# Kernel tuning notes

Measured on AMD Instinct MI355X. Metric: run time of the kernel, lower is better.

Reference implementation:

```python
import jax, jax.numpy as jnp
import numpy as np

N = 50000      # nodes
E = 800000     # edges (avg degree 16)
IN = 128       # in_channels
OUT = 200      # out_channels


def setup_inputs() -> dict:
    key = jax.random.key(0)
    ks = jax.random.split(key, 12)
    x = jax.random.normal(ks[0], (N, IN), dtype=jnp.float32)
    src = jax.random.randint(ks[1], (E,), 0, N, dtype=jnp.int32)
    off = jax.random.randint(ks[2], (E,), 1, N, dtype=jnp.int32)
    dst = (src + off) % N  # guarantees no self-loops (PyG ChebConv removes them)
    edge_index = jnp.stack([src, dst])
    edge_weight = jax.random.uniform(ks[3], (E,), dtype=jnp.float32) + 0.1
    s = 0.05
    # scale_1 (K=1): one weight; scale_2 (K=2): two; scale_3 (K=3): three. Biases per scale.
    return {
        "x": x,
        "edge_index": edge_index,
        "edge_weight": edge_weight,
        "w1_0": jax.random.normal(ks[4], (IN, OUT), dtype=jnp.float32) * s,
        "b1": jnp.zeros((OUT,), dtype=jnp.float32),
        "w2_0": jax.random.normal(ks[5], (IN, OUT), dtype=jnp.float32) * s,
        "w2_1": jax.random.normal(ks[6], (IN, OUT), dtype=jnp.float32) * s,
        "b2": jnp.zeros((OUT,), dtype=jnp.float32),
        "w3_0": jax.random.normal(ks[7], (IN, OUT), dtype=jnp.float32) * s,
        "w3_1": jax.random.normal(ks[8], (IN, OUT), dtype=jnp.float32) * s,
        "w3_2": jax.random.normal(ks[9], (IN, OUT), dtype=jnp.float32) * s,
        "b3": jnp.zeros((OUT,), dtype=jnp.float32),
    }


def _cheb_norm(edge_index, edge_weight, num_nodes):
    # PyG ChebConv.__norm__ with normalization='sym', lambda_max=2.0:
    # L = I - D^{-1/2} A D^{-1/2}; Lhat = 2L/lambda_max - I = -D^{-1/2} A D^{-1/2}
    # (self-loop weights become exactly 0, so we can drop them)
    row, col = edge_index[0], edge_index[1]
    deg = jax.ops.segment_sum(edge_weight, row, num_segments=num_nodes)
    dis = jnp.where(deg > 0, jax.lax.rsqrt(deg), 0.0)
    return -dis[row] * edge_weight * dis[col]


def _propagate(h, src, dst, norm, num_nodes):
    # out[i] = sum_{(j->i) in E} norm_e * h[j]
    return jax.ops.segment_sum(norm[:, None] * h[src], dst, num_segments=num_nodes)


def reference(x, edge_index, edge_weight, w1_0, b1, w2_0, w2_1, b2, w3_0, w3_1, w3_2, b3):
    num_nodes = x.shape[0]
    src, dst = edge_index[0], edge_index[1]
    norm = _cheb_norm(edge_index, edge_weight, num_nodes)
    # Chebyshev recursion (shared across the three scales; identical math):
    tx0 = x                                              # T_0(L) x
    tx1 = _propagate(tx0, src, dst, norm, num_nodes)     # T_1(L) x = Lhat x
    tx2 = 2.0 * _propagate(tx1, src, dst, norm, num_nodes) - tx0  # T_2(L) x
    s1 = tx0 @ w1_0 + b1
    s2 = tx0 @ w2_0 + tx1 @ w2_1 + b2
    s3 = tx0 @ w3_0 + tx1 @ w3_1 + tx2 @ w3_2 + b3
    return (s1, s2, s3)
```

## Files before the change

kernel.cpp:

```cpp
#include <hip/hip_runtime.h>

#define IN 128
#define OUT 200
#define NT 13
#define MT 64
#define RANGES 8
#define REPLICAS 64
#define RBMAX 6272

typedef __bf16 bf16x8 __attribute__((ext_vector_type(8)));
typedef float f32x4 __attribute__((ext_vector_type(4)));
typedef unsigned short ushort;
typedef ushort ushort8 __attribute__((ext_vector_type(8)));
typedef unsigned int uint;

__device__ inline ushort f2bf(float f) {
  uint b = __float_as_uint(f);
  return (ushort)((b + 0x7FFFu + ((b >> 16) & 1u)) >> 16);
}
__device__ inline float bf_lo(uint v) { return __uint_as_float(v << 16); }
__device__ inline float bf_hi(uint v) { return __uint_as_float(v & 0xFFFF0000u); }

__device__ inline size_t pk_idx(int row, int ch) {
  int rt = row >> 4, lr = row & 15, kk = ch >> 5, hi = (ch & 31) >> 3;
  return ((size_t)(rt * 4 + kk) * 64 + hi * 16 + lr) * 8 + (ch & 7);
}

__device__ inline void gload16(const void* g, void* l) {
  __builtin_amdgcn_global_load_lds(
      (const __attribute__((address_space(1))) void*)g,
      (__attribute__((address_space(3))) void*)l, 16, 0, 0);
}


__global__ __launch_bounds__(256) void k_hist(
    const int* __restrict__ src, const int* __restrict__ dst,
    const float* __restrict__ w, float* __restrict__ deg_part,
    int* __restrict__ cnt_part, int E, int N, int RB, int SL) {
  __shared__ float degL[RBMAX];
  __shared__ int cntL[RBMAX];
  int range = blockIdx.x / REPLICAS;
  int rep = blockIdx.x % REPLICAS;
  int base = range * RB;
  int lim = min(N - base, RB);
  for (int i = threadIdx.x; i < RB; i += 256) { degL[i] = 0.f; cntL[i] = 0; }
  __syncthreads();
  int e0 = rep * SL, e1 = min(E, e0 + SL);
  for (int e = e0 + (int)threadIdx.x; e < e1; e += 256) {
    int s = src[e], d = dst[e];
    int sl = s - base, dl = d - base;
    if ((unsigned)sl < (unsigned)lim) atomicAdd(&degL[sl], w[e]);
    if ((unsigned)dl < (unsigned)lim) atomicAdd(&cntL[dl], 1);
  }
  __syncthreads();
  for (int i = threadIdx.x; i < lim; i += 256) {
    deg_part[(size_t)rep * N + base + i] = degL[i];
    cnt_part[(size_t)rep * N + base + i] = cntL[i];
  }
}

__global__ void k_dis_scan(const float* __restrict__ deg_part, int* __restrict__ cnt_part,
                           float* __restrict__ dis,
                           int* __restrict__ offs, int* __restrict__ bsum, int n) {
  __shared__ int s[256];
  int t = threadIdx.x;
  int i = blockIdx.x * 256 + t;
  int v = 0;
  if (i < n) {
    float d = 0.f;
    int run = 0;
    for (int c = 0; c < REPLICAS; ++c) {
      size_t idx = (size_t)c * n + i;
      int cv = cnt_part[idx];
      cnt_part[idx] = run;
      run += cv;
      d += deg_part[idx];
    }
    v = run;
    dis[i] = d > 0.f ? rsqrtf(d) : 0.f;
  }
  s[t] = v;
  __syncthreads();
  for (int o = 1; o < 256; o <<= 1) {
    int a = (t >= o) ? s[t - o] : 0;
    __syncthreads();
    s[t] += a;
    __syncthreads();
  }
  if (i < n) offs[i] = s[t] - v;
  if (t == 255) bsum[blockIdx.x] = s[255];
}

__global__ void k_scan_c2(int* __restrict__ offs, const int* __restrict__ bsum,
                          int n, int E) {
  __shared__ int red[256];
  int t = threadIdx.x;
  int partial = 0;
  for (int i = t; i < (int)blockIdx.x; i += 256) partial += bsum[i];
  red[t] = partial;
  __syncthreads();
  for (int o = 128; o > 0; o >>= 1) {
    if (t < o) red[t] += red[t + o];
    __syncthreads();
  }
  int base = red[0];
  int i = blockIdx.x * 256 + t;
  if (i < n) offs[i] += base;
  if (i == 0) offs[n] = E;
}

__global__ __launch_bounds__(256) void k_fill(
    const int* __restrict__ src, const int* __restrict__ dst,
    const float* __restrict__ w, const float* __restrict__ dis,
    const int* __restrict__ offs, const int* __restrict__ pref,
    int2* __restrict__ csr_rec, int E, int N, int RB, int SL) {
  __shared__ int curL[RBMAX];
  int range = blockIdx.x / REPLICAS;
  int rep = blockIdx.x % REPLICAS;
  int base = range * RB;
  int lim = min(N - base, RB);
  for (int i = threadIdx.x; i < RB; i += 256) curL[i] = 0;
  __syncthreads();
  int e0 = rep * SL, e1 = min(E, e0 + SL);
  for (int e = e0 + (int)threadIdx.x; e < e1; e += 256) {
    int d = dst[e];
    int dl = d - base;
    if ((unsigned)dl < (unsigned)lim) {
      int s = src[e];
      int r = atomicAdd(&curL[dl], 1);
      int pos = offs[d] + pref[(size_t)rep * N + d] + r;
      float nm = -dis[s] * w[e] * dis[d];
      csr_rec[pos] = make_int2(s, __float_as_int(nm));
    }
  }
}


__global__ void k_cast_pack(const float* __restrict__ x, ushort* __restrict__ xb,
                            ushort* __restrict__ xp, int cast_blocks, long totx,
                            const float* __restrict__ w10, const float* __restrict__ w20,
                            const float* __restrict__ w21, const float* __restrict__ w30,
                            const float* __restrict__ w31, const float* __restrict__ w32,
                            ushort* __restrict__ wpack) {
  if (blockIdx.x < (unsigned)cast_blocks) {
    long i = ((long)blockIdx.x * blockDim.x + threadIdx.x) * 8;
    if (i >= totx) return;
    float4 a = *(const float4*)&x[i];
    float4 b = *(const float4*)&x[i + 4];
    ushort8 o;
    o[0] = f2bf(a.x); o[1] = f2bf(a.y); o[2] = f2bf(a.z); o[3] = f2bf(a.w);
    o[4] = f2bf(b.x); o[5] = f2bf(b.y); o[6] = f2bf(b.z); o[7] = f2bf(b.w);
    *(ushort8*)&xb[i] = o;
    int row = (int)(i >> 7), ch = (int)(i & 127);
    *(ushort8*)&xp[pk_idx(row, ch)] = o;
  } else {
    int gid = (blockIdx.x - cast_blocks) * blockDim.x + threadIdx.x;
    int total = 6 * NT * 4 * 64;
    if (gid >= total) return;
    int lane = gid & 63;
    int f = gid >> 6;
    int kk = f & 3;
    int g2 = f >> 2;
    int m = g2 % 6;
    int t = g2 / 6;
    const float* w = (m == 0) ? w10 : (m == 1) ? w20 : (m == 2) ? w21
                   : (m == 3) ? w30 : (m == 4) ? w31 : w32;
    int col = t * 16 + (lane & 15);
    int kbase = kk * 32 + (lane >> 4) * 8;
    ushort8 o;
#pragma unroll
    for (int j = 0; j < 8; ++j)
      o[j] = (col < OUT) ? f2bf(w[(kbase + j) * OUT + col]) : (ushort)0;
    *(ushort8*)&wpack[(size_t)gid * 8] = o;
  }
}


template <int MODE>
__global__ void k_gather(const ushort* __restrict__ h, const ushort* __restrict__ xb,
                         const int2* __restrict__ csr_rec,
                         const int* __restrict__ offs, ushort* __restrict__ out_lin,
                         ushort* __restrict__ out_pk, int n) {
  int node = blockIdx.x * 4 + (threadIdx.x >> 6);
  if (node >= n) return;
  int lane = threadIdx.x & 63;
  int ch0 = lane * 2;
  int s = offs[node], e = offs[node + 1];
  float lo[8], hi[8];
#pragma unroll
  for (int q = 0; q < 8; ++q) { lo[q] = 0.f; hi[q] = 0.f; }
  int p = s;
  for (; p + 7 < e; p += 8) {
    int2 rec[8]; uint v[8];
#pragma unroll
    for (int q = 0; q < 8; ++q) rec[q] = csr_rec[p + q];
#pragma unroll
    for (int q = 0; q < 8; ++q) v[q] = *(const uint*)&h[(size_t)rec[q].x * IN + ch0];
#pragma unroll
    for (int q = 0; q < 8; ++q) {
      float nm = __int_as_float(rec[q].y);
      lo[q] = fmaf(nm, bf_lo(v[q]), lo[q]);
      hi[q] = fmaf(nm, bf_hi(v[q]), hi[q]);
    }
  }
  for (; p + 1 < e; p += 2) {
    int2 r0 = csr_rec[p], r1 = csr_rec[p + 1];
    uint v0 = *(const uint*)&h[(size_t)r0.x * IN + ch0];
    uint v1 = *(const uint*)&h[(size_t)r1.x * IN + ch0];
    float n0 = __int_as_float(r0.y), n1 = __int_as_float(r1.y);
    lo[0] = fmaf(n0, bf_lo(v0), lo[0]); hi[0] = fmaf(n0, bf_hi(v0), hi[0]);
    lo[1] = fmaf(n1, bf_lo(v1), lo[1]); hi[1] = fmaf(n1, bf_hi(v1), hi[1]);
  }
  if (p < e) {
    int2 r0 = csr_rec[p];
    float n0 = __int_as_float(r0.y);
    uint v0 = *(const uint*)&h[(size_t)r0.x * IN + ch0];
    lo[2] = fmaf(n0, bf_lo(v0), lo[2]); hi[2] = fmaf(n0, bf_hi(v0), hi[2]);
  }
  float r0 = ((lo[0] + lo[1]) + (lo[2] + lo[3])) + ((lo[4] + lo[5]) + (lo[6] + lo[7]));
  float r1 = ((hi[0] + hi[1]) + (hi[2] + hi[3])) + ((hi[4] + hi[5]) + (hi[6] + hi[7]));
  if (MODE == 1) {
    uint xv = *(const uint*)&xb[(size_t)node * IN + ch0];
    r0 = 2.f * r0 - bf_lo(xv);
    r1 = 2.f * r1 - bf_hi(xv);
  }
  uint packed = (uint)f2bf(r0) | ((uint)f2bf(r1) << 16);
  if (MODE == 0)
    *(uint*)&out_lin[(size_t)node * IN + ch0] = packed;
  *(uint*)&out_pk[pk_idx(node, ch0)] = packed;
}


template <int NM, int CH0>
__device__ __forceinline__ void gemm_pass(
    const bf16x8 (&a)[3][4], const ushort* __restrict__ wpack,
    ushort (&bsm)[2][12 * 512], float (&st)[MT][212],
    const float* __restrict__ bias, float* __restrict__ outm,
    int n, int lane, int wave, int blk) {
  auto stage = [&](int t, int buf) {
    const ushort* src = wpack + ((size_t)t * 24 + CH0) * 512;
#pragma unroll
    for (int j = 0; j < NM; ++j) {
      int c = wave * NM + j;
      gload16(src + (size_t)c * 512 + (size_t)lane * 8, &bsm[buf][c * 512]);
    }
  };
  stage(0, 0);
  asm volatile("s_waitcnt vmcnt(0)" ::: "memory");
  __builtin_amdgcn_s_barrier();

  f32x4 acc[NT];
#pragma unroll
  for (int t = 0; t < NT; ++t) {
    int col = t * 16 + (lane & 15);
    float bb = bias[min(col, OUT - 1)];
    acc[t] = (f32x4){bb, bb, bb, bb};
  }

  int cur = 0;
#pragma unroll
  for (int t = 0; t < NT; ++t) {
    if (t + 1 < NT) stage(t + 1, cur ^ 1);
    const ushort* bb_ = &bsm[cur][0];
#pragma unroll
    for (int kk = 0; kk < 4; ++kk) {
#pragma unroll
      for (int mm = 0; mm < NM; ++mm) {
        bf16x8 b = __builtin_bit_cast(bf16x8,
            *(const ushort8*)&bb_[(mm * 4 + kk) * 512 + lane * 8]);
        acc[t] = __builtin_amdgcn_mfma_f32_16x16x32_bf16(a[mm][kk], b, acc[t], 0, 0, 0);
      }
    }
    asm volatile("s_waitcnt vmcnt(0)" ::: "memory");
    __builtin_amdgcn_s_barrier();
    cur ^= 1;
  }

  int rbase = wave * 16 + (lane >> 4) * 4;
#pragma unroll
  for (int t = 0; t < NT; ++t) {
    int c = t * 16 + (lane & 15);
#pragma unroll
    for (int r = 0; r < 4; ++r) st[rbase + r][c] = acc[t][r];
  }
#pragma unroll
  for (int r = 0; r < 16; ++r) {
    int lrow = wave * 16 + r;
    long grow = (long)blk * MT + lrow;
    if (grow < n && lane < 50) {
      float4 v = *(const float4*)&st[lrow][lane * 4];
      *(float4*)&outm[grow * OUT + lane * 4] = v;
    }
  }
}

__global__ __launch_bounds__(256) void k_gemm_mfma(
    const ushort* __restrict__ xp, const ushort* __restrict__ t1p, const ushort* __restrict__ t2p,
    const ushort* __restrict__ wpack,
    const float* __restrict__ b1v, const float* __restrict__ b2v, const float* __restrict__ b3v,
    float* __restrict__ out, int n) {
  __shared__ ushort bsm[2][12 * 512];
  __shared__ float st[MT][212];
  int lane = threadIdx.x & 63;
  int wave = threadIdx.x >> 6;
  int blk = blockIdx.x;
  int rt = (blk * MT + wave * 16) >> 4;

  bf16x8 a[3][4];
  const ushort* mats[3] = {xp, t1p, t2p};
#pragma unroll
  for (int m = 0; m < 3; ++m) {
#pragma unroll
    for (int kk = 0; kk < 4; ++kk) {
      size_t fi = ((size_t)rt * 4 + kk) * 512 + (size_t)lane * 8;
      a[m][kk] = __builtin_bit_cast(bf16x8, *(const ushort8*)&mats[m][fi]);
    }
  }
#pragma unroll
  for (int m = 0; m < 3; ++m)
#pragma unroll
    for (int kk = 0; kk < 4; ++kk)
      asm volatile("" : "+v"(a[m][kk]));

  long NS = (long)n * OUT;
  gemm_pass<1, 0>(a, wpack, bsm, st, b1v, out, n, lane, wave, blk);
  gemm_pass<2, 4>(a, wpack, bsm, st, b2v, out + NS, n, lane, wave, blk);
  gemm_pass<3, 12>(a, wpack, bsm, st, b3v, out + 2 * NS, n, lane, wave, blk);
}


extern "C" void kernel_launch(void* const* d_in, const int* in_sizes, int n_in,
                              void* d_out, int out_size, void* d_ws, size_t ws_size,
                              hipStream_t stream) {
  const float* x   = (const float*)d_in[0];
  const int*   ei  = (const int*)d_in[1];
  const float* ew  = (const float*)d_in[2];
  const float* w10 = (const float*)d_in[3];
  const float* b1  = (const float*)d_in[4];
  const float* w20 = (const float*)d_in[5];
  const float* w21 = (const float*)d_in[6];
  const float* b2  = (const float*)d_in[7];
  const float* w30 = (const float*)d_in[8];
  const float* w31 = (const float*)d_in[9];
  const float* w32 = (const float*)d_in[10];
  const float* b3  = (const float*)d_in[11];
  float* out = (float*)d_out;

  int N = in_sizes[0] / IN;
  int E = in_sizes[2];
  const int* src = ei;
  const int* dst = ei + E;

  int mtiles = (N + MT - 1) / MT;
  size_t prow = (size_t)mtiles * MT;
  size_t pksz = prow * IN * 2;

  int RB = (N + RANGES - 1) / RANGES;
  int SL = (E + REPLICAS - 1) / REPLICAS;

  char* ws = (char*)d_ws;
  size_t off = 0;
  auto alloc = [&](size_t bytes) {
    void* p = ws + off;
    off = (off + bytes + 15) & ~(size_t)15;
    return p;
  };
  float* deg_part = (float*)alloc((size_t)REPLICAS * N * 4);
  int*   cnt_part = (int*)alloc((size_t)REPLICAS * N * 4);
  float* dis      = (float*)alloc((size_t)N * 4);
  int*   offs     = (int*)alloc(((size_t)N + 1) * 4);
  int2*  csr_rec  = (int2*)alloc((size_t)E * 8);
  int*   bsum     = (int*)alloc(256 * 4);
  ushort* xb      = (ushort*)alloc((size_t)N * IN * 2);
  ushort* tx1b    = (ushort*)alloc((size_t)N * IN * 2);
  ushort* xp      = (ushort*)alloc(pksz);
  ushort* t1p     = (ushort*)alloc(pksz);
  ushort* t2p     = (ushort*)alloc(pksz);
  ushort* wpack   = (ushort*)alloc((size_t)6 * NT * 4 * 64 * 8 * 2);

  const int tb = 256;
  int nb = (N + 255) / 256;

  long totx = (long)N * IN;
  int cast_blocks = (int)((totx / 8 + tb - 1) / tb);
  int wp_blocks = (6 * NT * 4 * 64 + tb - 1) / tb;

  k_hist<<<RANGES * REPLICAS, 256, 0, stream>>>(src, dst, ew, deg_part, cnt_part, E, N, RB, SL);
  k_dis_scan<<<nb, 256, 0, stream>>>(deg_part, cnt_part, dis, offs, bsum, N);
  k_scan_c2<<<nb, 256, 0, stream>>>(offs, bsum, N, E);
  k_fill<<<RANGES * REPLICAS, 256, 0, stream>>>(src, dst, ew, dis, offs, cnt_part, csr_rec, E, N, RB, SL);
  k_cast_pack<<<cast_blocks + wp_blocks, tb, 0, stream>>>(
      x, xb, xp, cast_blocks, totx, w10, w20, w21, w30, w31, w32, wpack);

  int gblk = (N + 3) / 4;
  k_gather<0><<<gblk, 256, 0, stream>>>(xb, xb, csr_rec, offs, tx1b, t1p, N);
  k_gather<1><<<gblk, 256, 0, stream>>>(tx1b, xb, csr_rec, offs, nullptr, t2p, N);

  k_gemm_mfma<<<mtiles, 256, 0, stream>>>(xp, t1p, t2p, wpack, b1, b2, b3, out, N);
}
```

Baseline: 252.1 us.

## Split GEMM per scale and co-schedule scale GEMMs with gather kernels

Merges the x/weight cast-pack work into the histogram kernel and splits the single three-scale GEMM into per-scale pieces. The scale-1 GEMM now runs in the same launch as the first gather, scale 2 with the second gather, and only scale 3 runs alone. This is meant to overlap compute-bound MFMA work with the memory-bound gathers and remove launches. In exchange, the scale-1 and scale-2 GEMMs read weights straight from global memory without LDS staging and write output with uncoalesced scalar stores, and the A tiles are loaded again in each kernel.

```diff
diff --git a/kernel.cpp b/kernel.cpp
--- a/kernel.cpp
+++ b/kernel.cpp
@@ -33,31 +33,73 @@
 }
 
 
-__global__ __launch_bounds__(256) void k_hist(
+__global__ __launch_bounds__(256) void k_hist_cast(
     const int* __restrict__ src, const int* __restrict__ dst,
     const float* __restrict__ w, float* __restrict__ deg_part,
-    int* __restrict__ cnt_part, int E, int N, int RB, int SL) {
+    int* __restrict__ cnt_part, int E, int N, int RB, int SL,
+    const float* __restrict__ x, ushort* __restrict__ xb, ushort* __restrict__ xp,
+    int cast_blocks, long totx,
+    const float* __restrict__ w10, const float* __restrict__ w20,
+    const float* __restrict__ w21, const float* __restrict__ w30,
+    const float* __restrict__ w31, const float* __restrict__ w32,
+    ushort* __restrict__ wpack) {
   __shared__ float degL[RBMAX];
   __shared__ int cntL[RBMAX];
-  int range = blockIdx.x / REPLICAS;
-  int rep = blockIdx.x % REPLICAS;
-  int base = range * RB;
-  int lim = min(N - base, RB);
-  for (int i = threadIdx.x; i < RB; i += 256) { degL[i] = 0.f; cntL[i] = 0; }
-  __syncthreads();
-  int e0 = rep * SL, e1 = min(E, e0 + SL);
-  for (int e = e0 + (int)threadIdx.x; e < e1; e += 256) {
-    int s = src[e], d = dst[e];
-    int sl = s - base, dl = d - base;
-    if ((unsigned)sl < (unsigned)lim) atomicAdd(&degL[sl], w[e]);
-    if ((unsigned)dl < (unsigned)lim) atomicAdd(&cntL[dl], 1);
-  }
-  __syncthreads();
-  for (int i = threadIdx.x; i < lim; i += 256) {
-    deg_part[(size_t)rep * N + base + i] = degL[i];
-    cnt_part[(size_t)rep * N + base + i] = cntL[i];
-  }
-}
+  if (blockIdx.x < RANGES * REPLICAS) {
+    int range = blockIdx.x / REPLICAS;
+    int rep = blockIdx.x % REPLICAS;
+    int base = range * RB;
+    int lim = min(N - base, RB);
+    for (int i = threadIdx.x; i < RB; i += 256) { degL[i] = 0.f; cntL[i] = 0; }
+    __syncthreads();
+    int e0 = rep * SL, e1 = min(E, e0 + SL);
+    for (int e = e0 + (int)threadIdx.x; e < e1; e += 256) {
+      int s = src[e], d = dst[e];
+      int sl = s - base, dl = d - base;
+      if ((unsigned)sl < (unsigned)lim) atomicAdd(&degL[sl], w[e]);
+      if ((unsigned)dl < (unsigned)lim) atomicAdd(&cntL[dl], 1);
+    }
+    __syncthreads();
+    for (int i = threadIdx.x; i < lim; i += 256) {
+      deg_part[(size_t)rep * N + base + i] = degL[i];
+      cnt_part[(size_t)rep * N + base + i] = cntL[i];
+    }
+  } else {
+    int cid = blockIdx.x - RANGES * REPLICAS;
+    if (cid < cast_blocks) {
+      long i = ((long)cid * 256 + threadIdx.x) * 8;
+      if (i >= totx) return;
+      float4 a = *(const float4*)&x[i];
+      float4 b = *(const float4*)&x[i + 4];
+      ushort8 o;
+      o[0] = f2bf(a.x); o[1] = f2bf(a.y); o[2] = f2bf(a.z); o[3] = f2bf(a.w);
+      o[4] = f2bf(b.x); o[5] = f2bf(b.y); o[6] = f2bf(b.z); o[7] = f2bf(b.w);
+      *(ushort8*)&xb[i] = o;
+      int row = (int)(i >> 7), ch = (int)(i & 127);
+      *(ushort8*)&xp[pk_idx(row, ch)] = o;
+    } else {
+      int gid = (cid - cast_blocks) * 256 + threadIdx.x;
+      int total = 6 * NT * 4 * 64;
+      if (gid >= total) return;
+      int lane = gid & 63;
+      int f = gid >> 6;
+      int kk = f & 3;
+      int g2 = f >> 2;
+      int m = g2 % 6;
+      int t = g2 / 6;
+      const float* wq = (m == 0) ? w10 : (m == 1) ? w20 : (m == 2) ? w21
+                      : (m == 3) ? w30 : (m == 4) ? w31 : w32;
+      int col = t * 16 + (lane & 15);
+      int kbase = kk * 32 + (lane >> 4) * 8;
+      ushort8 o;
+#pragma unroll
+      for (int j = 0; j < 8; ++j)
+        o[j] = (col < OUT) ? f2bf(wq[(kbase + j) * OUT + col]) : (ushort)0;
+      *(ushort8*)&wpack[(((size_t)t * 24 + m * 4 + kk) * 64 + lane) * 8] = o;
+    }
+  }
+}
+
 
 __global__ void k_dis_scan(const float* __restrict__ deg_part, int* __restrict__ cnt_part,
                            float* __restrict__ dis,
@@ -136,52 +178,12 @@
 }
 
 
-__global__ void k_cast_pack(const float* __restrict__ x, ushort* __restrict__ xb,
-                            ushort* __restrict__ xp, int cast_blocks, long totx,
-                            const float* __restrict__ w10, const float* __restrict__ w20,
-                            const float* __restrict__ w21, const float* __restrict__ w30,
-                            const float* __restrict__ w31, const float* __restrict__ w32,
-                            ushort* __restrict__ wpack) {
-  if (blockIdx.x < (unsigned)cast_blocks) {
-    long i = ((long)blockIdx.x * blockDim.x + threadIdx.x) * 8;
-    if (i >= totx) return;
-    float4 a = *(const float4*)&x[i];
-    float4 b = *(const float4*)&x[i + 4];
-    ushort8 o;
-    o[0] = f2bf(a.x); o[1] = f2bf(a.y); o[2] = f2bf(a.z); o[3] = f2bf(a.w);
-    o[4] = f2bf(b.x); o[5] = f2bf(b.y); o[6] = f2bf(b.z); o[7] = f2bf(b.w);
-    *(ushort8*)&xb[i] = o;
-    int row = (int)(i >> 7), ch = (int)(i & 127);
-    *(ushort8*)&xp[pk_idx(row, ch)] = o;
-  } else {
-    int gid = (blockIdx.x - cast_blocks) * blockDim.x + threadIdx.x;
-    int total = 6 * NT * 4 * 64;
-    if (gid >= total) return;
-    int lane = gid & 63;
-    int f = gid >> 6;
-    int kk = f & 3;
-    int g2 = f >> 2;
-    int m = g2 % 6;
-    int t = g2 / 6;
-    const float* w = (m == 0) ? w10 : (m == 1) ? w20 : (m == 2) ? w21
-                   : (m == 3) ? w30 : (m == 4) ? w31 : w32;
-    int col = t * 16 + (lane & 15);
-    int kbase = kk * 32 + (lane >> 4) * 8;
-    ushort8 o;
-#pragma unroll
-    for (int j = 0; j < 8; ++j)
-      o[j] = (col < OUT) ? f2bf(w[(kbase + j) * OUT + col]) : (ushort)0;
-    *(ushort8*)&wpack[(size_t)gid * 8] = o;
-  }
-}
-
-
 template <int MODE>
-__global__ void k_gather(const ushort* __restrict__ h, const ushort* __restrict__ xb,
-                         const int2* __restrict__ csr_rec,
-                         const int* __restrict__ offs, ushort* __restrict__ out_lin,
-                         ushort* __restrict__ out_pk, int n) {
-  int node = blockIdx.x * 4 + (threadIdx.x >> 6);
+__device__ __forceinline__ void gather_body(
+    int gb, const ushort* __restrict__ h, const ushort* __restrict__ xb,
+    const int2* __restrict__ csr_rec, const int* __restrict__ offs,
+    ushort* __restrict__ out_lin, ushort* __restrict__ out_pk, int n) {
+  int node = gb * 4 + ((int)threadIdx.x >> 6);
   if (node >= n) return;
   int lane = threadIdx.x & 63;
   int ch0 = lane * 2;
@@ -232,16 +234,116 @@
 
 
 template <int NM, int CH0>
-__device__ __forceinline__ void gemm_pass(
-    const bf16x8 (&a)[3][4], const ushort* __restrict__ wpack,
-    ushort (&bsm)[2][12 * 512], float (&st)[MT][212],
-    const float* __restrict__ bias, float* __restrict__ outm,
-    int n, int lane, int wave, int blk) {
+__device__ __forceinline__ void gemm_direct(
+    const ushort* __restrict__ m0, const ushort* __restrict__ m1,
+    const ushort* __restrict__ wpack, const float* __restrict__ bias,
+    float* __restrict__ outm, int n, int blk) {
+  int lane = threadIdx.x & 63;
+  int wave = (int)threadIdx.x >> 6;
+  int row0 = blk * MT + wave * 16;
+  int rt = row0 >> 4;
+  const ushort* mats[2] = {m0, m1};
+  bf16x8 a[NM][4];
+#pragma unroll
+  for (int m = 0; m < NM; ++m)
+#pragma unroll
+    for (int kk = 0; kk < 4; ++kk) {
+      size_t fi = ((size_t)rt * 4 + kk) * 512 + (size_t)lane * 8;
+      a[m][kk] = __builtin_bit_cast(bf16x8, *(const ushort8*)&mats[m][fi]);
+    }
+#pragma unroll
+  for (int m = 0; m < NM; ++m)
+#pragma unroll
+    for (int kk = 0; kk < 4; ++kk)
+      asm volatile("" : "+v"(a[m][kk]));
+
+  for (int t = 0; t < NT; ++t) {
+    int col = t * 16 + (lane & 15);
+    bool colok = col < OUT;
+    float bb = bias[colok ? col : 0];
+    f32x4 acc = {bb, bb, bb, bb};
+#pragma unroll
+    for (int mm = 0; mm < NM; ++mm) {
+      const ushort* base = wpack + (((size_t)t * 24 + CH0 + mm * 4) * 64 + lane) * 8;
+      bf16x8 b0 = __builtin_bit_cast(bf16x8, *(const ushort8*)&base[0 * 512]);
+      bf16x8 b1 = __builtin_bit_cast(bf16x8, *(const ushort8*)&base[1 * 512]);
+      bf16x8 b2 = __builtin_bit_cast(bf16x8, *(const ushort8*)&base[2 * 512]);
+      bf16x8 b3 = __builtin_bit_cast(bf16x8, *(const ushort8*)&base[3 * 512]);
+      acc = __builtin_amdgcn_mfma_f32_16x16x32_bf16(a[mm][0], b0, acc, 0, 0, 0);
+      acc = __builtin_amdgcn_mfma_f32_16x16x32_bf16(a[mm][1], b1, acc, 0, 0, 0);
+      acc = __builtin_amdgcn_mfma_f32_16x16x32_bf16(a[mm][2], b2, acc, 0, 0, 0);
+      acc = __builtin_amdgcn_mfma_f32_16x16x32_bf16(a[mm][3], b3, acc, 0, 0, 0);
+    }
+    if (colok) {
+      int rbase = row0 + (lane >> 4) * 4;
+#pragma unroll
+      for (int r = 0; r < 4; ++r) {
+        int ra = rbase + r;
+        if (ra < n) outm[(long)ra * OUT + col] = acc[r];
+      }
+    }
+  }
+}
+
+
+__global__ __launch_bounds__(256, 5) void k_g1s1(
+    const ushort* __restrict__ xb, const ushort* __restrict__ xp,
+    const int2* __restrict__ csr_rec, const int* __restrict__ offs,
+    ushort* __restrict__ tx1b, ushort* __restrict__ t1p,
+    const ushort* __restrict__ wpack, const float* __restrict__ b1v,
+    float* __restrict__ out1, int n, int GB) {
+  if ((int)blockIdx.x < GB)
+    gemm_direct<1, 0>(xp, nullptr, wpack, b1v, out1, n, blockIdx.x);
+  else
+    gather_body<0>(blockIdx.x - GB, xb, xb, csr_rec, offs, tx1b, t1p, n);
+}
+
+
+__global__ __launch_bounds__(256, 5) void k_g2s2(
+    const ushort* __restrict__ xb, const ushort* __restrict__ tx1b,
+    const ushort* __restrict__ xp, const ushort* __restrict__ t1p,
+    const int2* __restrict__ csr_rec, const int* __restrict__ offs,
+    ushort* __restrict__ t2p,
+    const ushort* __restrict__ wpack, const float* __restrict__ b2v,
+    float* __restrict__ out2, int n, int GB) {
+  if ((int)blockIdx.x < GB)
+    gemm_direct<2, 4>(xp, t1p, wpack, b2v, out2, n, blockIdx.x);
+  else
+    gather_body<1>(blockIdx.x - GB, tx1b, xb, csr_rec, offs, nullptr, t2p, n);
+}
+
+
+__global__ __launch_bounds__(256) void k_s3(
+    const ushort* __restrict__ xp, const ushort* __restrict__ t1p, const ushort* __restrict__ t2p,
+    const ushort* __restrict__ wpack, const float* __restrict__ b3v,
+    float* __restrict__ out3, int n) {
+  __shared__ ushort bsm[2][12 * 512];
+  __shared__ float st[MT][212];
+  int lane = threadIdx.x & 63;
+  int wave = (int)threadIdx.x >> 6;
+  int blk = blockIdx.x;
+  int rt = (blk * MT + wave * 16) >> 4;
+
+  bf16x8 a[3][4];
+  const ushort* mats[3] = {xp, t1p, t2p};
+#pragma unroll
+  for (int m = 0; m < 3; ++m)
+#pragma unroll
+    for (int kk = 0; kk < 4; ++kk) {
+      size_t fi = ((size_t)rt * 4 + kk) * 512 + (size_t)lane * 8;
+      a[m][kk] = __builtin_bit_cast(bf16x8, *(const ushort8*)&mats[m][fi]);
+    }
+#pragma unroll
+  for (int m = 0; m < 3; ++m)
+#pragma unroll
+    for (int kk = 0; kk < 4; ++kk)
+      asm volatile("" : "+v"(a[m][kk]));
+
   auto stage = [&](int t, int buf) {
-    const ushort* src = wpack + ((size_t)t * 24 + CH0) * 512;
-#pragma unroll
-    for (int j = 0; j < NM; ++j) {
-      int c = wave * NM + j;
+    const ushort* src = wpack + ((size_t)t * 24 + 12) * 512;
+#pragma unroll
+    for (int j = 0; j < 3; ++j) {
+      int c = wave * 3 + j;
       gload16(src + (size_t)c * 512 + (size_t)lane * 8, &bsm[buf][c * 512]);
     }
   };
@@ -253,7 +355,7 @@
 #pragma unroll
   for (int t = 0; t < NT; ++t) {
     int col = t * 16 + (lane & 15);
-    float bb = bias[min(col, OUT - 1)];
+    float bb = b3v[min(col, OUT - 1)];
     acc[t] = (f32x4){bb, bb, bb, bb};
   }
 
@@ -265,7 +367,7 @@
 #pragma unroll
     for (int kk = 0; kk < 4; ++kk) {
 #pragma unroll
-      for (int mm = 0; mm < NM; ++mm) {
+      for (int mm = 0; mm < 3; ++mm) {
         bf16x8 b = __builtin_bit_cast(bf16x8,
             *(const ushort8*)&bb_[(mm * 4 + kk) * 512 + lane * 8]);
         acc[t] = __builtin_amdgcn_mfma_f32_16x16x32_bf16(a[mm][kk], b, acc[t], 0, 0, 0);
@@ -289,43 +391,9 @@
     long grow = (long)blk * MT + lrow;
     if (grow < n && lane < 50) {
       float4 v = *(const float4*)&st[lrow][lane * 4];
-      *(float4*)&outm[grow * OUT + lane * 4] = v;
-    }
-  }
-}
-
-__global__ __launch_bounds__(256) void k_gemm_mfma(
-    const ushort* __restrict__ xp, const ushort* __restrict__ t1p, const ushort* __restrict__ t2p,
-    const ushort* __restrict__ wpack,
-    const float* __restrict__ b1v, const float* __restrict__ b2v, const float* __restrict__ b3v,
-    float* __restrict__ out, int n) {
-  __shared__ ushort bsm[2][12 * 512];
-  __shared__ float st[MT][212];
-  int lane = threadIdx.x & 63;
-  int wave = threadIdx.x >> 6;
-  int blk = blockIdx.x;
-  int rt = (blk * MT + wave * 16) >> 4;
-
-  bf16x8 a[3][4];
-  const ushort* mats[3] = {xp, t1p, t2p};
-#pragma unroll
-  for (int m = 0; m < 3; ++m) {
-#pragma unroll
-    for (int kk = 0; kk < 4; ++kk) {
-      size_t fi = ((size_t)rt * 4 + kk) * 512 + (size_t)lane * 8;
-      a[m][kk] = __builtin_bit_cast(bf16x8, *(const ushort8*)&mats[m][fi]);
-    }
-  }
-#pragma unroll
-  for (int m = 0; m < 3; ++m)
-#pragma unroll
-    for (int kk = 0; kk < 4; ++kk)
-      asm volatile("" : "+v"(a[m][kk]));
-
-  long NS = (long)n * OUT;
-  gemm_pass<1, 0>(a, wpack, bsm, st, b1v, out, n, lane, wave, blk);
-  gemm_pass<2, 4>(a, wpack, bsm, st, b2v, out + NS, n, lane, wave, blk);
-  gemm_pass<3, 12>(a, wpack, bsm, st, b3v, out + 2 * NS, n, lane, wave, blk);
+      *(float4*)&out3[grow * OUT + lane * 4] = v;
+    }
+  }
 }
 
 
@@ -378,23 +446,30 @@
   ushort* t2p     = (ushort*)alloc(pksz);
   ushort* wpack   = (ushort*)alloc((size_t)6 * NT * 4 * 64 * 8 * 2);
 
-  const int tb = 256;
   int nb = (N + 255) / 256;
 
   long totx = (long)N * IN;
-  int cast_blocks = (int)((totx / 8 + tb - 1) / tb);
-  int wp_blocks = (6 * NT * 4 * 64 + tb - 1) / tb;
-
-  k_hist<<<RANGES * REPLICAS, 256, 0, stream>>>(src, dst, ew, deg_part, cnt_part, E, N, RB, SL);
+  int cast_blocks = (int)((totx / 8 + 255) / 256);
+  int wp_blocks = (6 * NT * 4 * 64 + 255) / 256;
+  int HB = RANGES * REPLICAS;
+
+  long NS = (long)N * OUT;
+  float* out1 = out;
+  float* out2 = out + NS;
+  float* out3 = out + 2 * NS;
+
+  int gblk = (N + 3) / 4;
+
+  k_hist_cast<<<HB + cast_blocks + wp_blocks, 256, 0, stream>>>(
+      src, dst, ew, deg_part, cnt_part, E, N, RB, SL,
+      x, xb, xp, cast_blocks, totx, w10, w20, w21, w30, w31, w32, wpack);
   k_dis_scan<<<nb, 256, 0, stream>>>(deg_part, cnt_part, dis, offs, bsum, N);
   k_scan_c2<<<nb, 256, 0, stream>>>(offs, bsum, N, E);
-  k_fill<<<RANGES * REPLICAS, 256, 0, stream>>>(src, dst, ew, dis, offs, cnt_part, csr_rec, E, N, RB, SL);
-  k_cast_pack<<<cast_blocks + wp_blocks, tb, 0, stream>>>(
-      x, xb, xp, cast_blocks, totx, w10, w20, w21, w30, w31, w32, wpack);
-
-  int gblk = (N + 3) / 4;
-  k_gather<0><<<gblk, 256, 0, stream>>>(xb, xb, csr_rec, offs, tx1b, t1p, N);
-  k_gather<1><<<gblk, 256, 0, stream>>>(tx1b, xb, csr_rec, offs, nullptr, t2p, N);
-
-  k_gemm_mfma<<<mtiles, 256, 0, stream>>>(xp, t1p, t2p, wpack, b1, b2, b3, out, N);
-}
+  k_fill<<<HB, 256, 0, stream>>>(src, dst, ew, dis, offs, cnt_part, csr_rec, E, N, RB, SL);
+
+  k_g1s1<<<mtiles + gblk, 256, 0, stream>>>(
+      xb, xp, csr_rec, offs, tx1b, t1p, wpack, b1, out1, N, mtiles);
+  k_g2s2<<<mtiles + gblk, 256, 0, stream>>>(
+      xb, tx1b, xp, t1p, csr_rec, offs, t2p, wpack, b2, out2, N, mtiles);
+  k_s3<<<mtiles, 256, 0, stream>>>(xp, t1p, t2p, wpack, b3, out3, N);
+}
```

Result: faster. 239.5 us (-5.0%).
